# Optimization experiments

Hardware: AMD Instinct MI355X
Metric: run time of the kernel (lower is better)

## Reference

```python
import jax, jax.numpy as jnp
import numpy as np

LN_EPS = 1e-5

def conv2d(x, w, b, padding, dilation=1):
    # x: [B,C,H,W], w: [O,I,kh,kw] (torch OIHW layout)
    y = jax.lax.conv_general_dilated(
        x, w, window_strides=(1, 1),
        padding=[(padding, padding), (padding, padding)],
        rhs_dilation=(dilation, dilation),
        dimension_numbers=('NCHW', 'OIHW', 'NCHW'))
    return y + b[None, :, None, None]

def layer_norm(x, w, b):
    # normalize over (C,H,W) like nn.LayerNorm([C,15,15])
    mu = jnp.mean(x, axis=(1, 2, 3), keepdims=True)
    var = jnp.var(x, axis=(1, 2, 3), keepdims=True)
    return (x - mu) * jax.lax.rsqrt(var + LN_EPS) * w[None] + b[None]

def setup_inputs() -> dict:
    key = jax.random.key(0)
    B, C, H, W, S = 256, 256, 15, 15, 8
    ks = jax.random.split(key, 20)
    def w_conv(k, kh, kw):
        fan_in = C * kh * kw
        bound = 1.0 / np.sqrt(fan_in)
        return jax.random.uniform(k, (C, C, kh, kw), jnp.float32, -bound, bound)
    def w_fusion(k):
        fan_in = 4 * C
        bound = 1.0 / np.sqrt(fan_in)
        return jax.random.uniform(k, (C, 4 * C, 1, 1), jnp.float32, -bound, bound)
    def bias(k, fan_in, n=None):
        bound = 1.0 / np.sqrt(fan_in)
        return jax.random.uniform(k, (n if n is not None else C,), jnp.float32, -bound, bound)
    return {
        'x': jax.random.normal(ks[0], (B, C, H, W), jnp.float32),
        'spiking_probabilities': jax.random.uniform(ks[1], (S,), jnp.float32),
        'w3': w_conv(ks[2], 3, 3), 'b3': bias(ks[3], C * 9),
        'w3d': w_conv(ks[4], 3, 3), 'b3d': bias(ks[5], C * 9),
        'w5': w_conv(ks[6], 5, 5), 'b5': bias(ks[7], C * 25),
        'w7': w_conv(ks[8], 7, 7), 'b7': bias(ks[9], C * 49),
        'wf': w_fusion(ks[10]), 'bf': bias(ks[11], 4 * C),
        'w1': w_conv(ks[12], 1, 1), 'b1': bias(ks[13], C),
        'ln_w': jnp.ones((C, H, W), jnp.float32),
        'ln_b': jnp.zeros((C, H, W), jnp.float32),
        'step_param': jax.random.uniform(ks[14], (S,), jnp.float32),
        'spike_scale': jax.random.uniform(ks[15], (S,), jnp.float32),
        'residual_weights': jax.random.uniform(ks[16], (S,), jnp.float32),
    }

def reference(x, spiking_probabilities, w3, b3, w3d, b3d, w5, b5, w7, b7,
              wf, bf, w1, b1, ln_w, ln_b, step_param, spike_scale, residual_weights):
    elu = jax.nn.elu
    # multi-scale perception
    dx3 = elu(conv2d(x, w3, b3, padding=1))
    dx3d = elu(conv2d(x, w3d, b3d, padding=2, dilation=2))
    dx5 = elu(conv2d(x, w5, b5, padding=2))
    dx7 = elu(conv2d(x, w7, b7, padding=3))
    xf = elu(conv2d(jnp.concatenate([dx3, dx3d, dx5, dx7], axis=1), wf, bf, padding=0))

    base_key = jax.random.key(42)
    num_steps = step_param.shape[0]

    def step(xc, inp):
        sp, ss, rw, prob, i = inp
        dx = elu(layer_norm(conv2d(xc, w1, b1, padding=0), ln_w, ln_b))
        v = jnp.var(dx, axis=(1, 2, 3), ddof=1)  # torch.var unbiased
        noise = jax.random.uniform(jax.random.fold_in(base_key, i), xc.shape, xc.dtype)
        x_new = xc + dx * sp + noise * prob * ss + xc * rw
        return x_new, v

    xs = (step_param, spike_scale, residual_weights,
          spiking_probabilities, jnp.arange(num_steps))
    x_final, vs = jax.lax.scan(step, xf, xs)
    nca_var = vs.T  # [B, num_steps]
    return (x_final, nca_var)
```

## Files before the change

### kernel.cpp

```cpp
#include <hip/hip_runtime.h>
#include <cstdint>

constexpr int B_ = 256, C_ = 256, H_ = 15, W_ = 15, P_ = 225, S_ = 8;
constexpr int CHW = C_ * P_;
constexpr size_t NX = (size_t)B_ * CHW;

typedef __attribute__((ext_vector_type(8))) short short8v;
typedef __attribute__((ext_vector_type(4))) float float4v;
typedef __attribute__((ext_vector_type(16))) float float16v;

__host__ __device__ inline void tf2x32(uint32_t k0, uint32_t k1,
                                       uint32_t x0, uint32_t x1,
                                       uint32_t& o0, uint32_t& o1) {
  uint32_t ks[3] = {k0, k1, k0 ^ k1 ^ 0x1BD11BDAu};
  const uint32_t rot0[4] = {13u, 15u, 26u, 6u};
  const uint32_t rot1[4] = {17u, 29u, 16u, 24u};
  x0 += ks[0]; x1 += ks[1];
#pragma unroll
  for (int r = 0; r < 5; ++r) {
    const uint32_t* rr = (r & 1) ? rot1 : rot0;
#pragma unroll
    for (int j = 0; j < 4; ++j) {
      x0 += x1;
      x1 = (x1 << rr[j]) | (x1 >> (32 - rr[j]));
      x1 ^= x0;
    }
    x0 += ks[(r + 1) % 3];
    x1 += ks[(r + 2) % 3] + (uint32_t)(r + 1);
  }
  o0 = x0; o1 = x1;
}

__device__ inline float tf_uniform(uint32_t bits) {
  return __uint_as_float((bits >> 9) | 0x3F800000u) - 1.0f;
}

__device__ inline float elu1(float v) { return v > 0.f ? v : expm1f(v); }

__device__ inline unsigned short f2bf(float f) {
  uint32_t u = __float_as_uint(f);
  return (unsigned short)((u + 0x7FFFu + ((u >> 16) & 1u)) >> 16);
}
__device__ inline float bf2f(unsigned short h) {
  return __uint_as_float(((uint32_t)h) << 16);
}

template <int KS, int DIL, int OFF>
__global__ void __launch_bounds__(256, 2) conv_mfma(
    const unsigned short* __restrict__ xbf, const unsigned short* __restrict__ wt,
    const float* __restrict__ bias, unsigned short* __restrict__ dxg) {
  constexpr int KS2 = KS * KS, HP = H_ + 2 * OFF, WP = 23, PP = WP * HP;
  constexpr int NCH = (KS2 + 2) / 3;
  __shared__ __align__(16) unsigned short lsA[4 * PP * 8];
  __shared__ __align__(16) unsigned short lsB[2][3 * 4 * 128 * 8];
  const int b = blockIdx.x, nh = blockIdx.y;
  const int t = threadIdx.x, wv = t >> 6, l = t & 63;
  const int m32 = l & 31, kh8 = l >> 5;
  for (int i = t; i < 4 * PP * 8; i += 256) lsA[i] = 0;
  int rbase[2];
#pragma unroll
  for (int mt = 0; mt < 2; ++mt) {
    int m = (wv * 2 + mt) * 32 + m32;
    int pc = m < P_ ? m : P_ - 1;
    int ph = pc / 15, pw = pc - 15 * ph;
    rbase[mt] = ph * WP + pw;
  }
  float16v acc[2][4];
#pragma unroll
  for (int mt = 0; mt < 2; ++mt)
#pragma unroll
    for (int nt = 0; nt < 4; ++nt)
#pragma unroll
      for (int r = 0; r < 16; ++r) acc[mt][nt][r] = 0.f;
  const unsigned short* xb = xbf + (size_t)b * P_ * 256;
  const int brow = t & 63, bpl = t >> 6;
  const unsigned short* wbase = wt + nh * 4096;
  __syncthreads();
  for (int i = t; i < 900; i += 256) {
    int pl = i / 225, p = i - 225 * pl;
    short8v v = *(const short8v*)(xb + p * 256 + pl * 8);
    int ph = p / 15, pw = p - 15 * ph;
    *(short8v*)&lsA[(pl * PP + (ph + OFF) * WP + pw + OFF) * 8] = v;
  }
#pragma unroll
  for (int j = 0; j < 3; ++j) {
    short8v v0 = *(const short8v*)(wbase + (size_t)j * 8192 + brow * 32 + bpl * 8);
    short8v v1 = *(const short8v*)(wbase + (size_t)j * 8192 + (brow + 64) * 32 + bpl * 8);
    *(short8v*)&lsB[0][((j * 4 + bpl) * 128 + brow) * 8] = v0;
    *(short8v*)&lsB[0][((j * 4 + bpl) * 128 + 64 + brow) * 8] = v1;
  }
  __syncthreads();
  for (int chk = 0; chk < 8 * NCH; ++chk) {
    const int cb = chk / NCH;
    const int c0 = (chk - cb * NCH) * 3;
    const int dn = (KS2 - c0) < 3 ? (KS2 - c0) : 3;
    const int cur = chk & 1;
    const bool hasNext = (chk + 1) < 8 * NCH;
    const int ncb = (chk + 1) / NCH;
    const int nc0 = ((chk + 1) - ncb * NCH) * 3;
    const int ndn = hasNext ? ((KS2 - nc0) < 3 ? (KS2 - nc0) : 3) : 0;
    const bool cross = hasNext && (ncb != cb);
    short8v nb0[3], nb1[3];
    if (hasNext) {
      const unsigned short* wn = wbase + ((size_t)ncb * KS2 + nc0) * 8192;
#pragma unroll
      for (int j = 0; j < 3; ++j)
        if (j < ndn) {
          nb0[j] = *(const short8v*)(wn + (size_t)j * 8192 + brow * 32 + bpl * 8);
          nb1[j] = *(const short8v*)(wn + (size_t)j * 8192 + (brow + 64) * 32 + bpl * 8);
        }
    }
    auto mfma_d = [&](int dd) {
      const int d = c0 + dd;
      const int kh = d / KS, kw = d - KS * kh;
      const int doff = DIL * (kh * WP + kw);
      const unsigned short* bb = lsB[cur] + dd * 4096;
#pragma unroll
      for (int k16 = 0; k16 < 2; ++k16) {
        const int pl = k16 * 2 + kh8;
        short8v af[2], bfr[4];
#pragma unroll
        for (int mt = 0; mt < 2; ++mt)
          af[mt] = *(const short8v*)&lsA[(pl * PP + rbase[mt] + doff) * 8];
#pragma unroll
        for (int nt = 0; nt < 4; ++nt)
          bfr[nt] = *(const short8v*)&bb[(pl * 128 + nt * 32 + m32) * 8];
#pragma unroll
        for (int mt = 0; mt < 2; ++mt)
#pragma unroll
          for (int nt = 0; nt < 4; ++nt)
            acc[mt][nt] = __builtin_amdgcn_mfma_f32_32x32x16_bf16(
                af[mt], bfr[nt], acc[mt][nt], 0, 0, 0);
      }
    };
    __builtin_amdgcn_s_setprio(1);
    mfma_d(0);
    if (dn == 3) { mfma_d(1); mfma_d(2); }
    __builtin_amdgcn_s_setprio(0);
    if (hasNext) {
      unsigned short* bw = lsB[cur ^ 1];
#pragma unroll
      for (int j = 0; j < 3; ++j)
        if (j < ndn) {
          *(short8v*)&bw[((j * 4 + bpl) * 128 + brow) * 8] = nb0[j];
          *(short8v*)&bw[((j * 4 + bpl) * 128 + 64 + brow) * 8] = nb1[j];
        }
    }
    __syncthreads();
    if (cross) {
      for (int i = t; i < 900; i += 256) {
        int pl = i / 225, p = i - 225 * pl;
        short8v v = *(const short8v*)(xb + p * 256 + ncb * 32 + pl * 8);
        int ph = p / 15, pw = p - 15 * ph;
        *(short8v*)&lsA[(pl * PP + (ph + OFF) * WP + pw + OFF) * 8] = v;
      }
      __syncthreads();
    }
  }
#pragma unroll
  for (int nt = 0; nt < 4; ++nt) {
    int o = nh * 128 + nt * 32 + m32;
    float bv = bias[o];
#pragma unroll
    for (int mt = 0; mt < 2; ++mt) {
#pragma unroll
      for (int r = 0; r < 16; ++r) {
        int pixel = (wv * 2 + mt) * 32 + 8 * (r >> 2) + (r & 3) + 4 * kh8;
        if (pixel < P_)
          dxg[((size_t)(b * P_ + pixel)) * 256 + o] = f2bf(elu1(acc[mt][nt][r] + bv));
      }
    }
  }
}

__global__ void __launch_bounds__(512, 4) gemm_kc(
    const unsigned short* __restrict__ A0, const unsigned short* __restrict__ A1,
    const float* __restrict__ Af, int nkb,
    const unsigned short* __restrict__ Bw, const float* __restrict__ bias,
    float* __restrict__ xc, unsigned short* __restrict__ ybf,
    float* __restrict__ stats, int mode) {
  __shared__ __align__(16) unsigned short lsA[4 * P_ * 8];
  __shared__ __align__(16) unsigned short lsB[4 * 128 * 8];
  __shared__ float red[16];
  const int b = blockIdx.x, nh = blockIdx.y;
  const int t = threadIdx.x, wv = t >> 6, l = t & 63;
  const int m32 = l & 31, kh8 = l >> 5;
  const int mp = wv & 3, nq = wv >> 2;
  int prow[2];
#pragma unroll
  for (int mt = 0; mt < 2; ++mt) {
    int m = (mp * 2 + mt) * 32 + m32;
    prow[mt] = m < P_ ? m : P_ - 1;
  }
  float16v acc[2][2];
#pragma unroll
  for (int mt = 0; mt < 2; ++mt)
#pragma unroll
    for (int nt = 0; nt < 2; ++nt)
#pragma unroll
      for (int r = 0; r < 16; ++r) acc[mt][nt][r] = 0.f;
  const float* Afb = Af ? Af + (size_t)b * P_ * 256 : nullptr;
  const int brow = t & 127, bpl = t >> 7;
  for (int kb = 0; kb < nkb; ++kb) {
    __syncthreads();
    if (Af) {
      for (int i = t; i < 900; i += 512) {
        int pl = i / 225, p = i - 225 * pl;
        const float* src = Afb + (size_t)p * 256 + kb * 32 + pl * 8;
        float4v f0 = *(const float4v*)src;
        float4v f1 = *(const float4v*)(src + 4);
        short8v v;
        v[0] = (short)f2bf(f0[0]); v[1] = (short)f2bf(f0[1]);
        v[2] = (short)f2bf(f0[2]); v[3] = (short)f2bf(f0[3]);
        v[4] = (short)f2bf(f1[0]); v[5] = (short)f2bf(f1[1]);
        v[6] = (short)f2bf(f1[2]); v[7] = (short)f2bf(f1[3]);
        *(short8v*)&lsA[(pl * P_ + p) * 8] = v;
      }
    } else {
      const unsigned short* Asb =
          ((kb & 8) ? A1 : A0) + (size_t)b * P_ * 256;
      for (int i = t; i < 900; i += 512) {
        int pl = i / 225, p = i - 225 * pl;
        short8v v = *(const short8v*)(Asb + (size_t)p * 256 + (kb & 7) * 32 + pl * 8);
        *(short8v*)&lsA[(pl * P_ + p) * 8] = v;
      }
    }
    {
      short8v v = *(const short8v*)(Bw + (size_t)kb * 8192 + nh * 4096 + brow * 32 + bpl * 8);
      *(short8v*)&lsB[(bpl * 128 + brow) * 8] = v;
    }
    __syncthreads();
#pragma unroll
    for (int k16 = 0; k16 < 2; ++k16) {
      const int pl = k16 * 2 + kh8;
      short8v af[2], bfr[2];
#pragma unroll
      for (int mt = 0; mt < 2; ++mt)
        af[mt] = *(const short8v*)&lsA[(pl * P_ + prow[mt]) * 8];
#pragma unroll
      for (int nt = 0; nt < 2; ++nt)
        bfr[nt] = *(const short8v*)&lsB[(pl * 128 + (nq * 2 + nt) * 32 + m32) * 8];
#pragma unroll
      for (int mt = 0; mt < 2; ++mt)
#pragma unroll
        for (int nt = 0; nt < 2; ++nt)
          acc[mt][nt] = __builtin_amdgcn_mfma_f32_32x32x16_bf16(
              af[mt], bfr[nt], acc[mt][nt], 0, 0, 0);
    }
  }
  float s1 = 0.f, s2 = 0.f;
#pragma unroll
  for (int nt = 0; nt < 2; ++nt) {
    int o = nh * 128 + (nq * 2 + nt) * 32 + m32;
    float bv = bias ? bias[o] : 0.f;
#pragma unroll
    for (int mt = 0; mt < 2; ++mt) {
#pragma unroll
      for (int r = 0; r < 16; ++r) {
        int pixel = (mp * 2 + mt) * 32 + 8 * (r >> 2) + (r & 3) + 4 * kh8;
        if (pixel >= P_) continue;
        size_t idx = ((size_t)(b * P_ + pixel)) * 256 + o;
        float v = acc[mt][nt][r];
        if (mode == 0) {
          xc[idx] = v;
        } else if (mode == 2) {
          xc[idx] = elu1(xc[idx] + v + bv);
        } else {
          v += bv;
          ybf[idx] = f2bf(v);
          s1 += v;
          s2 = fmaf(v, v, s2);
        }
      }
    }
  }
  if (mode == 3) {
#pragma unroll
    for (int off = 32; off; off >>= 1) {
      s1 += __shfl_down(s1, off, 64);
      s2 += __shfl_down(s2, off, 64);
    }
    if (l == 0) { red[wv] = s1; red[8 + wv] = s2; }
    __syncthreads();
    if (t == 0) {
      float a = 0.f, c2 = 0.f;
#pragma unroll
      for (int w = 0; w < 8; ++w) { a += red[w]; c2 += red[8 + w]; }
      stats[nh * 512 + b] = a;
      stats[nh * 512 + 256 + b] = c2;
    }
  }
}

__global__ void __launch_bounds__(512) step_fused(
    const unsigned short* __restrict__ ybf, float* __restrict__ xc,
    unsigned short* __restrict__ xcbf, const float* __restrict__ stats,
    const float* __restrict__ lnwT, const float* __restrict__ lnbT,
    const float* __restrict__ sp_a, const float* __restrict__ ss_a,
    const float* __restrict__ rw_a, const float* __restrict__ prob_a,
    int s, uint32_t k0, uint32_t k1, int last, float* __restrict__ vout) {
  __shared__ float red[16];
  const int b = blockIdx.x, t = threadIdx.x;
  const float mean = (stats[b] + stats[512 + b]) * (1.0f / 57600.0f);
  const float var =
      (stats[256 + b] + stats[768 + b]) * (1.0f / 57600.0f) - mean * mean;
  const float rstd = rsqrtf(var + 1e-5f);
  const float sp = sp_a[s], pss = prob_a[s] * ss_a[s], rw1 = 1.0f + rw_a[s];
  float s1 = 0.f, s2 = 0.f;
  const size_t base = (size_t)b * CHW;
  for (int g = t; g < 7200; g += 512) {
    int i0 = g * 8;
    int p = i0 >> 8, c0 = i0 & 255;
    size_t idx = base + i0;
    short8v yv = *(const short8v*)(ybf + idx);
    float4v x0 = *(const float4v*)(xc + idx);
    float4v x1 = *(const float4v*)(xc + idx + 4);
    float4v lw0 = *(const float4v*)(lnwT + i0);
    float4v lw1 = *(const float4v*)(lnwT + i0 + 4);
    float4v lb0 = *(const float4v*)(lnbT + i0);
    float4v lb1 = *(const float4v*)(lnbT + i0 + 4);
    const uint32_t jbase = (uint32_t)b * 57600u + (uint32_t)c0 * 225u + (uint32_t)p;
    float4v o0, o1;
    short8v ob;
#pragma unroll
    for (int e = 0; e < 8; ++e) {
      float y = bf2f((unsigned short)yv[e]);
      float lw = e < 4 ? lw0[e] : lw1[e - 4];
      float lb = e < 4 ? lb0[e] : lb1[e - 4];
      float xo = e < 4 ? x0[e] : x1[e - 4];
      float dx = elu1(fmaf((y - mean) * rstd, lw, lb));
      s1 += dx;
      s2 = fmaf(dx, dx, s2);
      uint32_t y0, y1;
      tf2x32(k0, k1, 0u, jbase + 225u * (uint32_t)e, y0, y1);
      float n = tf_uniform(y0 ^ y1);
      float xn = fmaf(xo, rw1, fmaf(dx, sp, n * pss));
      if (e < 4) o0[e] = xn; else o1[e - 4] = xn;
      ob[e] = (short)f2bf(xn);
    }
    *(float4v*)(xc + idx) = o0;
    *(float4v*)(xc + idx + 4) = o1;
    if (!last) *(short8v*)(xcbf + idx) = ob;
  }
  int wv = t >> 6, l = t & 63;
#pragma unroll
  for (int off = 32; off; off >>= 1) {
    s1 += __shfl_down(s1, off, 64);
    s2 += __shfl_down(s2, off, 64);
  }
  if (l == 0) { red[wv] = s1; red[8 + wv] = s2; }
  __syncthreads();
  if (t == 0) {
    float a = 0.f, c2 = 0.f;
#pragma unroll
    for (int w = 0; w < 8; ++w) { a += red[w]; c2 += red[8 + w]; }
    float mv = a * (1.0f / 57600.0f);
    vout[b * 8 + s] = (c2 - 57600.0f * mv * mv) * (1.0f / 57599.0f);
  }
}

__global__ void __launch_bounds__(256) prep_x(const float* __restrict__ x,
                                              unsigned short* __restrict__ xbf) {
  __shared__ unsigned short ts[64 * 232];
  const int b = blockIdx.x, c0 = blockIdx.y * 64;
  const float* xs = x + ((size_t)b * 256 + c0) * P_;
  for (int i = threadIdx.x; i < 64 * P_; i += 256) {
    int c = i / P_, p = i - P_ * c;
    ts[c * 232 + p] = f2bf(xs[c * P_ + p]);
  }
  __syncthreads();
  for (int i = threadIdx.x; i < 64 * P_; i += 256) {
    int p = i >> 6, c = i & 63;
    xbf[((size_t)b * P_ + p) * 256 + c0 + c] = ts[c * 232 + p];
  }
}

__global__ void wt_prep(const float* __restrict__ w, unsigned short* __restrict__ wt,
                        int ks2) {
  int i = blockIdx.x * 256 + threadIdx.x;
  if (i >= 65536 * ks2) return;
  int cl = i & 31, o = (i >> 5) & 255, cbd = i >> 13;
  int d = cbd % ks2, cb = cbd / ks2;
  wt[i] = f2bf(w[((size_t)(o * 256) + cb * 32 + cl) * ks2 + d]);
}

__global__ void wk_prep(const float* __restrict__ w, unsigned short* __restrict__ wt,
                        int K) {
  int i = blockIdx.x * 256 + threadIdx.x;
  if (i >= K * 256) return;
  int kc = i & 31, o = (i >> 5) & 255, kb = i >> 13;
  wt[i] = f2bf(w[(size_t)o * K + kb * 32 + kc]);
}

__global__ void ln_tr(const float* __restrict__ lw, const float* __restrict__ lb,
                      float* __restrict__ ow, float* __restrict__ ob) {
  int p = blockIdx.x, c = threadIdx.x;
  ow[p * 256 + c] = lw[c * P_ + p];
  ob[p * 256 + c] = lb[c * P_ + p];
}

__global__ void __launch_bounds__(256) final_tr(const float* __restrict__ xc,
                                                float* __restrict__ out) {
  __shared__ float ts[64][226];
  const int b = blockIdx.x, c0 = blockIdx.y * 64;
  for (int i = threadIdx.x; i < 64 * P_; i += 256) {
    int cl = i & 63, p = i >> 6;
    ts[cl][p] = xc[((size_t)(b * P_ + p)) * 256 + c0 + cl];
  }
  __syncthreads();
  for (int i = threadIdx.x; i < 64 * P_; i += 256) {
    int cl = i / P_, p = i - P_ * cl;
    out[((size_t)(b * 256 + c0 + cl)) * P_ + p] = ts[cl][p];
  }
}

extern "C" void kernel_launch(void* const* d_in, const int* in_sizes, int n_in,
                              void* d_out, int out_size, void* d_ws,
                              size_t ws_size, hipStream_t stream) {
  const float* x = (const float*)d_in[0];
  const float* prob = (const float*)d_in[1];
  const float* w3 = (const float*)d_in[2];
  const float* b3 = (const float*)d_in[3];
  const float* w3d = (const float*)d_in[4];
  const float* b3d = (const float*)d_in[5];
  const float* w5 = (const float*)d_in[6];
  const float* b5 = (const float*)d_in[7];
  const float* w7 = (const float*)d_in[8];
  const float* b7 = (const float*)d_in[9];
  const float* wf = (const float*)d_in[10];
  const float* bfus = (const float*)d_in[11];
  const float* w1 = (const float*)d_in[12];
  const float* b1 = (const float*)d_in[13];
  const float* lnw = (const float*)d_in[14];
  const float* lnb = (const float*)d_in[15];
  const float* sp = (const float*)d_in[16];
  const float* ss = (const float*)d_in[17];
  const float* rw = (const float*)d_in[18];
  float* out = (float*)d_out;

  unsigned short* dxg0 = (unsigned short*)d_ws;
  unsigned short* dxg1 = (unsigned short*)((char*)d_ws + 29491200);
  float* xc = (float*)((char*)d_ws + 58982400);
  unsigned short* xcbf = dxg0;
  unsigned short* ybf = dxg1;

  char* sc = (char*)d_out;
  unsigned short* wT3 = (unsigned short*)(sc + 0);
  unsigned short* wT3d = (unsigned short*)(sc + 1179648);
  unsigned short* wT5 = (unsigned short*)(sc + 2359296);
  unsigned short* wT7 = (unsigned short*)(sc + 5636096);
  unsigned short* wfT = (unsigned short*)(sc + 12058624);
  unsigned short* w1T = (unsigned short*)(sc + 12582912);
  float* lnwT = (float*)(sc + 12713984);
  float* lnbT = (float*)(sc + 12944384);
  unsigned short* xbf = (unsigned short*)(sc + 13174784);
  float* stats = (float*)(sc + 42665984);

  prep_x<<<dim3(B_, 4), 256, 0, stream>>>(x, xbf);
  wt_prep<<<(65536 * 9 + 255) / 256, 256, 0, stream>>>(w3, wT3, 9);
  wt_prep<<<(65536 * 9 + 255) / 256, 256, 0, stream>>>(w3d, wT3d, 9);
  wt_prep<<<(65536 * 25 + 255) / 256, 256, 0, stream>>>(w5, wT5, 25);
  wt_prep<<<(65536 * 49 + 255) / 256, 256, 0, stream>>>(w7, wT7, 49);
  wk_prep<<<1024, 256, 0, stream>>>(wf, wfT, 1024);
  wk_prep<<<256, 256, 0, stream>>>(w1, w1T, 256);
  ln_tr<<<P_, 256, 0, stream>>>(lnw, lnb, lnwT, lnbT);

  conv_mfma<3, 1, 1><<<dim3(B_, 2), 256, 0, stream>>>(xbf, wT3, b3, dxg0);
  conv_mfma<3, 2, 2><<<dim3(B_, 2), 256, 0, stream>>>(xbf, wT3d, b3d, dxg1);
  gemm_kc<<<dim3(B_, 2), 512, 0, stream>>>(dxg0, dxg1, nullptr, 16, wfT,
                                           nullptr, xc, nullptr, nullptr, 0);
  conv_mfma<5, 1, 2><<<dim3(B_, 2), 256, 0, stream>>>(xbf, wT5, b5, dxg0);
  conv_mfma<7, 1, 3><<<dim3(B_, 2), 256, 0, stream>>>(xbf, wT7, b7, dxg1);
  gemm_kc<<<dim3(B_, 2), 512, 0, stream>>>(dxg0, dxg1, nullptr, 16, wfT + 131072,
                                           bfus, xc, nullptr, nullptr, 2);

  gemm_kc<<<dim3(B_, 2), 512, 0, stream>>>(nullptr, nullptr, xc, 8, w1T, b1,
                                           nullptr, ybf, stats, 3);
  for (int si = 0; si < S_; ++si) {
    uint32_t k0s, k1s;
    tf2x32(0u, 42u, 0u, (uint32_t)si, k0s, k1s);
    step_fused<<<B_, 512, 0, stream>>>(ybf, xc, xcbf, stats, lnwT, lnbT, sp, ss, rw,
                                       prob, si, k0s, k1s, si == S_ - 1, out + NX);
    if (si < S_ - 1)
      gemm_kc<<<dim3(B_, 2), 512, 0, stream>>>(xcbf, xcbf, nullptr, 8, w1T, b1,
                                               nullptr, ybf, stats, 3);
  }

  final_tr<<<dim3(B_, 4), 256, 0, stream>>>(xc, out);
}
```

Before: 1.720 ms.

## Load conv weights straight to LDS and software-pipeline MFMA fragment loads

Weight tiles for the multi-scale conv kernel are now copied global-to-LDS with global_load_lds instead of being staged through registers, which frees registers and removes the explicit LDS store phase. The MFMA inner loop is restructured into a double-buffered fragment pipeline, so LDS reads for the next k-slice are issued while the current MFMAs run. LDS zero-init is also vectorized. A risk is that the LDS-direct loads need correct ordering relative to the barrier: there is no explicit wait for the async copy, and the per-lane destination layout depends on the M0/base semantics of global_load_lds.

Result: slower. 3.313 ms (+92.6%).

```diff
diff --git a/kernel.cpp b/kernel.cpp
--- a/kernel.cpp
+++ b/kernel.cpp
@@ -43,6 +43,12 @@
 }
 __device__ inline float bf2f(unsigned short h) {
   return __uint_as_float(((uint32_t)h) << 16);
+}
+
+__device__ inline void gload16(const unsigned short* g, unsigned short* l) {
+  __builtin_amdgcn_global_load_lds(
+      (__attribute__((address_space(1))) void*)(void*)(unsigned short*)(uintptr_t)(const unsigned short*)g,
+      (__attribute__((address_space(3))) void*)l, 16, 0, 0);
 }
 
 template <int KS, int DIL, int OFF>
@@ -56,7 +62,10 @@
   const int b = blockIdx.x, nh = blockIdx.y;
   const int t = threadIdx.x, wv = t >> 6, l = t & 63;
   const int m32 = l & 31, kh8 = l >> 5;
-  for (int i = t; i < 4 * PP * 8; i += 256) lsA[i] = 0;
+  {
+    short8v zz = {0, 0, 0, 0, 0, 0, 0, 0};
+    for (int i = t; i < 4 * PP; i += 256) *(short8v*)&lsA[i * 8] = zz;
+  }
   int rbase[2];
 #pragma unroll
   for (int mt = 0; mt < 2; ++mt) {
@@ -73,23 +82,24 @@
 #pragma unroll
       for (int r = 0; r < 16; ++r) acc[mt][nt][r] = 0.f;
   const unsigned short* xb = xbf + (size_t)b * P_ * 256;
+  const unsigned short* wbase = wt + nh * 4096;
   const int brow = t & 63, bpl = t >> 6;
-  const unsigned short* wbase = wt + nh * 4096;
   __syncthreads();
+#pragma unroll
+  for (int j = 0; j < 3; ++j) {
+    gload16(wbase + (size_t)j * 8192 + brow * 32 + bpl * 8,
+            &lsB[0][((j * 4 + bpl) * 128) * 8]);
+    gload16(wbase + (size_t)j * 8192 + (brow + 64) * 32 + bpl * 8,
+            &lsB[0][((j * 4 + bpl) * 128 + 64) * 8]);
+  }
   for (int i = t; i < 900; i += 256) {
     int pl = i / 225, p = i - 225 * pl;
     short8v v = *(const short8v*)(xb + p * 256 + pl * 8);
     int ph = p / 15, pw = p - 15 * ph;
     *(short8v*)&lsA[(pl * PP + (ph + OFF) * WP + pw + OFF) * 8] = v;
   }
-#pragma unroll
-  for (int j = 0; j < 3; ++j) {
-    short8v v0 = *(const short8v*)(wbase + (size_t)j * 8192 + brow * 32 + bpl * 8);
-    short8v v1 = *(const short8v*)(wbase + (size_t)j * 8192 + (brow + 64) * 32 + bpl * 8);
-    *(short8v*)&lsB[0][((j * 4 + bpl) * 128 + brow) * 8] = v0;
-    *(short8v*)&lsB[0][((j * 4 + bpl) * 128 + 64 + brow) * 8] = v1;
-  }
   __syncthreads();
+  short8v fA0[2], fB0[4], fA1[2], fB1[4];
   for (int chk = 0; chk < 8 * NCH; ++chk) {
     const int cb = chk / NCH;
     const int c0 = (chk - cb * NCH) * 3;
@@ -100,52 +110,53 @@
     const int nc0 = ((chk + 1) - ncb * NCH) * 3;
     const int ndn = hasNext ? ((KS2 - nc0) < 3 ? (KS2 - nc0) : 3) : 0;
     const bool cross = hasNext && (ncb != cb);
-    short8v nb0[3], nb1[3];
     if (hasNext) {
       const unsigned short* wn = wbase + ((size_t)ncb * KS2 + nc0) * 8192;
+      unsigned short* bw = lsB[cur ^ 1];
 #pragma unroll
       for (int j = 0; j < 3; ++j)
         if (j < ndn) {
-          nb0[j] = *(const short8v*)(wn + (size_t)j * 8192 + brow * 32 + bpl * 8);
-          nb1[j] = *(const short8v*)(wn + (size_t)j * 8192 + (brow + 64) * 32 + bpl * 8);
+          gload16(wn + (size_t)j * 8192 + brow * 32 + bpl * 8,
+                  &bw[((j * 4 + bpl) * 128) * 8]);
+          gload16(wn + (size_t)j * 8192 + (brow + 64) * 32 + bpl * 8,
+                  &bw[((j * 4 + bpl) * 128 + 64) * 8]);
         }
     }
-    auto mfma_d = [&](int dd) {
+    auto lfr = [&](short8v (&fa)[2], short8v (&fb)[4], int dd, int k16) {
       const int d = c0 + dd;
       const int kh = d / KS, kw = d - KS * kh;
       const int doff = DIL * (kh * WP + kw);
+      const int pl = k16 * 2 + kh8;
       const unsigned short* bb = lsB[cur] + dd * 4096;
 #pragma unroll
-      for (int k16 = 0; k16 < 2; ++k16) {
-        const int pl = k16 * 2 + kh8;
-        short8v af[2], bfr[4];
-#pragma unroll
-        for (int mt = 0; mt < 2; ++mt)
-          af[mt] = *(const short8v*)&lsA[(pl * PP + rbase[mt] + doff) * 8];
+      for (int mt = 0; mt < 2; ++mt)
+        fa[mt] = *(const short8v*)&lsA[(pl * PP + rbase[mt] + doff) * 8];
+#pragma unroll
+      for (int nt = 0; nt < 4; ++nt)
+        fb[nt] = *(const short8v*)&bb[(pl * 128 + nt * 32 + m32) * 8];
+    };
+    auto mf = [&](short8v (&fa)[2], short8v (&fb)[4]) {
+#pragma unroll
+      for (int mt = 0; mt < 2; ++mt)
 #pragma unroll
         for (int nt = 0; nt < 4; ++nt)
-          bfr[nt] = *(const short8v*)&bb[(pl * 128 + nt * 32 + m32) * 8];
-#pragma unroll
-        for (int mt = 0; mt < 2; ++mt)
-#pragma unroll
-          for (int nt = 0; nt < 4; ++nt)
-            acc[mt][nt] = __builtin_amdgcn_mfma_f32_32x32x16_bf16(
-                af[mt], bfr[nt], acc[mt][nt], 0, 0, 0);
-      }
+          acc[mt][nt] = __builtin_amdgcn_mfma_f32_32x32x16_bf16(
+              fa[mt], fb[nt], acc[mt][nt], 0, 0, 0);
     };
+    lfr(fA0, fB0, 0, 0);
     __builtin_amdgcn_s_setprio(1);
-    mfma_d(0);
-    if (dn == 3) { mfma_d(1); mfma_d(2); }
+    if (dn == 3) {
+      lfr(fA1, fB1, 0, 1); mf(fA0, fB0);
+      lfr(fA0, fB0, 1, 0); mf(fA1, fB1);
+      lfr(fA1, fB1, 1, 1); mf(fA0, fB0);
+      lfr(fA0, fB0, 2, 0); mf(fA1, fB1);
+      lfr(fA1, fB1, 2, 1); mf(fA0, fB0);
+      mf(fA1, fB1);
+    } else {
+      lfr(fA1, fB1, 0, 1); mf(fA0, fB0);
+      mf(fA1, fB1);
+    }
     __builtin_amdgcn_s_setprio(0);
-    if (hasNext) {
-      unsigned short* bw = lsB[cur ^ 1];
-#pragma unroll
-      for (int j = 0; j < 3; ++j)
-        if (j < ndn) {
-          *(short8v*)&bw[((j * 4 + bpl) * 128 + brow) * 8] = nb0[j];
-          *(short8v*)&bw[((j * 4 + bpl) * 128 + 64 + brow) * 8] = nb1[j];
-        }
-    }
     __syncthreads();
     if (cross) {
       for (int i = t; i < 900; i += 256) {
```
